# Kernel tuning notes

Measured on AMD Instinct MI355X. Metric: run time of the kernel, lower is better.

Reference implementation:

```python
import jax, jax.numpy as jnp
import numpy as np

B, L, D, O = 4, 256, 512, 128

def setup_inputs() -> dict:
    key = jax.random.key(0)
    k1, k2, k3, k4, k5, k6 = jax.random.split(key, 6)
    return {
        "x1": jax.random.normal(k1, (B, L, D), jnp.float32),
        "x2": jax.random.normal(k2, (B, L, D), jnp.float32),
        "bw": jax.random.uniform(k3, (2,), jnp.float32),
        "W_bil": jax.random.normal(k4, (O, D + 1, D + 1), jnp.float32) * 0.02,
        "W_lin": jax.random.normal(k5, (2 * D, O), jnp.float32) * 0.02,
        "b_lin": jax.random.normal(k6, (O,), jnp.float32) * 0.02,
    }

def reference(x1, x2, bw, W_bil, W_lin, b_lin):
    bwn = jax.nn.softmax(bw)
    d1 = x1.shape[-1]
    # Bilinear with bias_x/bias_y: append ones column to x1 and x2.
    ones1 = jnp.ones((*x1.shape[:2], 1), x1.dtype)
    ones2 = jnp.ones((*x2.shape[:2], 1), x2.dtype)
    x1b = jnp.concatenate([x1, ones1], axis=-1)  # [B, L1, D+1]
    x2b = jnp.concatenate([x2, ones2], axis=-1)  # [B, L2, D+1]
    # einsum 'bxi,oij,byj->boxy' then permute(0,2,3,1) -> bxyo
    bilinear_logits = jnp.einsum('bxi,oij,byj->bxyo', x1b, W_bil, x2b)
    # linear over concat([x1 expanded, x2 expanded]) == split-weight broadcast sum
    lin1 = x1 @ W_lin[:d1]   # [B, L1, O]
    lin2 = x2 @ W_lin[d1:]   # [B, L2, O]
    linear_logits = lin1[:, :, None, :] + lin2[:, None, :, :] + b_lin  # [B, L1, L2, O]
    return bwn[0] * bilinear_logits + bwn[1] * linear_logits
```

## Files before the change

### kernel.cpp

```cpp
#include <hip/hip_runtime.h>


#define LL 256
#define DD 512
#define OO 128
#define BB 4
#define WB_OI 263169
#define WB_R512 262656

typedef __attribute__((ext_vector_type(8))) short  short8;
typedef __attribute__((ext_vector_type(8))) unsigned short us8;
typedef __attribute__((ext_vector_type(4))) unsigned short us4;
typedef __attribute__((ext_vector_type(4))) float  f32x4;

__device__ __forceinline__ unsigned short f2bf(float f) {
    unsigned int u = __builtin_bit_cast(unsigned int, f);
    u = (u + 0x7FFFu + ((u >> 16) & 1u)) >> 16;
    return (unsigned short)u;
}
__device__ __forceinline__ float bf2f(unsigned short s) {
    return __builtin_bit_cast(float, (unsigned int)s << 16);
}
__device__ __forceinline__ void load_lds16(const void* g, void* l) {
    __builtin_amdgcn_global_load_lds(
        (const __attribute__((address_space(1))) unsigned int*)g,
        (__attribute__((address_space(3))) unsigned int*)l, 16, 0, 0);
}

__global__ __launch_bounds__(256) void cast_kernel(
    const float* __restrict__ src, unsigned short* __restrict__ dst, int n4)
{
    int i = blockIdx.x * 256 + threadIdx.x;
    if (i < n4) {
        float4 v = ((const float4*)src)[i];
        us4 u; u.x = f2bf(v.x); u.y = f2bf(v.y); u.z = f2bf(v.z); u.w = f2bf(v.w);
        *(us4*)(dst + (size_t)i * 4) = u;
    }
}

__global__ __launch_bounds__(256) void prepw_kernel(
    const float* __restrict__ Wb, const float* __restrict__ bw,
    unsigned short* __restrict__ Wb16)
{
    const int t = threadIdx.x;
    const int row = blockIdx.x * 4 + (t >> 6);
    const int o = row >> 9, i = row & 511;
    const int l = t & 63;
    const float e0 = __expf(bw[0]), e1 = __expf(bw[1]);
    const float bwn0 = e0 / (e0 + e1);
    const float* src = Wb + (size_t)o * WB_OI + (size_t)i * 513 + l * 8;
    float4 v0 = *(const float4*)src;
    float4 v1 = *(const float4*)(src + 4);
    us8 u;
    u[0] = f2bf(bwn0 * v0.x); u[1] = f2bf(bwn0 * v0.y);
    u[2] = f2bf(bwn0 * v0.z); u[3] = f2bf(bwn0 * v0.w);
    u[4] = f2bf(bwn0 * v1.x); u[5] = f2bf(bwn0 * v1.y);
    u[6] = f2bf(bwn0 * v1.z); u[7] = f2bf(bwn0 * v1.w);
    *(us8*)(Wb16 + (size_t)row * 512 + l * 8) = u;
}

__global__ __launch_bounds__(128) void u512_kernel(
    const float* __restrict__ x2, const float* __restrict__ Wb,
    const float* __restrict__ W_lin, const float* __restrict__ b_lin,
    const float* __restrict__ bw, float* __restrict__ u512buf)
{
    __shared__ float xs[DD];
    const int by = blockIdx.x;
    const int o  = threadIdx.x;
    const float* xr = x2 + (size_t)by * DD;
    for (int j = o; j < DD; j += 128) xs[j] = xr[j];
    __syncthreads();
    const float* W2 = Wb + (size_t)o * WB_OI + WB_R512;
    float s1 = W2[512];
    float s2 = b_lin[o];
    for (int j = 0; j < DD; ++j) {
        s1 += xs[j] * W2[j];
        s2 += xs[j] * W_lin[(size_t)(DD + j) * OO + o];
    }
    const float e0 = __expf(bw[0]), e1 = __expf(bw[1]);
    const float bwn0 = e0 / (e0 + e1), bwn1 = e1 / (e0 + e1);
    u512buf[(size_t)by * OO + o] = bwn0 * s1 + bwn1 * s2;
}

__global__ __launch_bounds__(256) void passA_kernel(
    const unsigned short* __restrict__ x2b, const unsigned short* __restrict__ Wb16,
    const float* __restrict__ W_bil, const float* __restrict__ W_lin,
    const float* __restrict__ bw, unsigned short* __restrict__ Up, int b)
{
    __shared__ __align__(16) char smem[18432];
    unsigned short* As = (unsigned short*)smem;
    unsigned short* Bs = (unsigned short*)(smem + 8192);
    unsigned short* Cs = (unsigned short*)smem;
    float* corr = (float*)(smem + 17408);

    const int t = threadIdx.x, w = t >> 6, l = t & 63;
    const int ib = blockIdx.x * 128;
    const int yb = blockIdx.y * 128;
    const int o  = blockIdx.z;
    const int wy = w & 1, wx = w >> 1;

    f32x4 acc[4][4] = {};
    const unsigned short* Wo16 = Wb16 + (size_t)o * DD * DD;

    for (int kt = 0; kt < 16; ++kt) {
        const int k0 = kt * 32;
        #pragma unroll
        for (int q = 0; q < 2; ++q) {
            const int rb = w * 32 + q * 16;
            const int rr = rb + (l >> 2);
            const int ko = k0 + (l & 3) * 8;
            load_lds16(x2b + (size_t)(b * LL + yb + rr) * DD + ko, As + rb * 32);
            load_lds16(Wo16 + (size_t)(ib + rr) * DD + ko, Bs + rb * 32);
        }
        __syncthreads();
        short8 af[4], bf[4];
        const int mrow = wy * 64 + (l & 15);
        const int ncol = wx * 64 + (l & 15);
        const int kg = (l >> 4) * 8;
        #pragma unroll
        for (int mt = 0; mt < 4; ++mt) af[mt] = *(const short8*)(As + (mrow + mt * 16) * 32 + kg);
        #pragma unroll
        for (int nt = 0; nt < 4; ++nt) bf[nt] = *(const short8*)(Bs + (ncol + nt * 16) * 32 + kg);
        #pragma unroll
        for (int mt = 0; mt < 4; ++mt)
            #pragma unroll
            for (int nt = 0; nt < 4; ++nt)
                acc[mt][nt] = __builtin_amdgcn_mfma_f32_16x16x32_bf16(af[mt], bf[nt], acc[mt][nt], 0, 0, 0);
        __syncthreads();
    }

    const float e0 = __expf(bw[0]), e1 = __expf(bw[1]);
    const float bwn0 = e0 / (e0 + e1), bwn1 = e1 / (e0 + e1);
    if (t < 128) {
        const int ig = ib + t;
        corr[t] = bwn1 * W_lin[(size_t)ig * OO + o]
                + bwn0 * W_bil[(size_t)o * WB_OI + (size_t)ig * 513 + 512];
    }
    #pragma unroll
    for (int half = 0; half < 2; ++half) {
        if (wy == half) {
            #pragma unroll
            for (int mt = 0; mt < 4; ++mt) {
                const int yl = mt * 16 + ((l >> 4) << 2);
                #pragma unroll
                for (int nt = 0; nt < 4; ++nt) {
                    const int ic = wx * 64 + nt * 16 + (l & 15);
                    #pragma unroll
                    for (int r = 0; r < 4; ++r)
                        Cs[(yl + r) * 136 + ic] = f2bf(acc[mt][nt][r]);
                }
            }
        }
        __syncthreads();
        #pragma unroll
        for (int p = 0; p < 4; ++p) {
            const int yl = p * 16 + (t >> 4);
            const int i0 = (t & 15) * 8;
            short8 v = *(const short8*)(Cs + yl * 136 + i0);
            us8 uo;
            #pragma unroll
            for (int e = 0; e < 8; ++e)
                uo[e] = f2bf(bf2f((unsigned short)v[e]) + corr[i0 + e]);
            *(us8*)(Up + ((size_t)(yb + half * 64 + yl) * OO + o) * DD + ib + i0) = uo;
        }
        __syncthreads();
    }
}

__global__ __launch_bounds__(256) void passB_kernel(
    const unsigned short* __restrict__ x1b, const unsigned short* __restrict__ Up,
    const float* __restrict__ u512buf, float* __restrict__ out, int b)
{
    __shared__ unsigned short As[128 * 32];
    __shared__ unsigned short Bs[128 * 32];
    __shared__ float u5[128];
    const int t = threadIdx.x, w = t >> 6, l = t & 63;
    const int xb = blockIdx.x * 128;
    const int y  = blockIdx.y;
    const int wy = w & 1, wx = w >> 1;
    if (t < 128) u5[t] = u512buf[(size_t)(b * LL + y) * OO + t];

    f32x4 acc[4][4] = {};

    for (int kt = 0; kt < 16; ++kt) {
        const int k0 = kt * 32;
        #pragma unroll
        for (int q = 0; q < 2; ++q) {
            const int rb = w * 32 + q * 16;
            const int rr = rb + (l >> 2);
            const int ko = k0 + (l & 3) * 8;
            load_lds16(x1b + (size_t)(b * LL + xb + rr) * DD + ko, As + rb * 32);
            load_lds16(Up + (size_t)(y * OO + rr) * DD + ko, Bs + rb * 32);
        }
        __syncthreads();
        short8 af[4], bf[4];
        const int mrow = wy * 64 + (l & 15);
        const int ncol = wx * 64 + (l & 15);
        const int kg = (l >> 4) * 8;
        #pragma unroll
        for (int mt = 0; mt < 4; ++mt) af[mt] = *(const short8*)(As + (mrow + mt * 16) * 32 + kg);
        #pragma unroll
        for (int nt = 0; nt < 4; ++nt) bf[nt] = *(const short8*)(Bs + (ncol + nt * 16) * 32 + kg);
        #pragma unroll
        for (int mt = 0; mt < 4; ++mt)
            #pragma unroll
            for (int nt = 0; nt < 4; ++nt)
                acc[mt][nt] = __builtin_amdgcn_mfma_f32_16x16x32_bf16(af[mt], bf[nt], acc[mt][nt], 0, 0, 0);
        __syncthreads();
    }

    #pragma unroll
    for (int mt = 0; mt < 4; ++mt) {
        const int xr = wy * 64 + mt * 16 + ((l >> 4) << 2);
        #pragma unroll
        for (int nt = 0; nt < 4; ++nt) {
            const int oc = wx * 64 + nt * 16 + (l & 15);
            const float c = u5[oc];
            #pragma unroll
            for (int r = 0; r < 4; ++r)
                out[((size_t)(b * LL + xb + xr + r) * LL + y) * OO + oc] = acc[mt][nt][r] + c;
        }
    }
}

extern "C" void kernel_launch(void* const* d_in, const int* in_sizes, int n_in,
                              void* d_out, int out_size, void* d_ws, size_t ws_size,
                              hipStream_t stream)
{
    const float* x1    = (const float*)d_in[0];
    const float* x2    = (const float*)d_in[1];
    const float* bw    = (const float*)d_in[2];
    const float* W_bil = (const float*)d_in[3];
    const float* W_lin = (const float*)d_in[4];
    const float* b_lin = (const float*)d_in[5];
    float* out = (float*)d_out;

    char* ws = (char*)d_ws;
    unsigned short* x1b16 = (unsigned short*)ws;
    unsigned short* x2b16 = (unsigned short*)(ws + (1u << 20));
    float*          u512b = (float*)(ws + (2u << 20));
    unsigned short* Wb16  = (unsigned short*)(ws + (3u << 20));
    unsigned short* Up    = (unsigned short*)(ws + (3u << 20) + ((size_t)128 * 512 * 512 * 2));

    cast_kernel<<<512, 256, 0, stream>>>(x1, x1b16, 131072);
    cast_kernel<<<512, 256, 0, stream>>>(x2, x2b16, 131072);
    prepw_kernel<<<16384, 256, 0, stream>>>(W_bil, bw, Wb16);
    u512_kernel<<<BB * LL, 128, 0, stream>>>(x2, W_bil, W_lin, b_lin, bw, u512b);

    for (int b = 0; b < BB; ++b) {
        passA_kernel<<<dim3(4, 2, OO), 256, 0, stream>>>(x2b16, Wb16, W_bil, W_lin, bw, Up, b);
        passB_kernel<<<dim3(2, LL), 256, 0, stream>>>(x1b16, Up, u512b, out, b);
    }
}
```

Baseline: 504.4 us.

## Batch passA/passB over all batches, double-buffer LDS, coalesce weight prep

Launches passA and passB once over all batches instead of looping per batch, which gives larger grids and removes per-batch launch serialization. Both GEMM kernels now double-buffer their LDS tiles so the next K-slice loads while the current one is multiplied. prepw uses coalesced scalar loads and stores instead of misaligned float4 loads, and the last-row bilinear weights are transposed once so u512 reads them coalesced. The two cast kernels are merged into one launch. In exchange the Up workspace grows to cover all batches, which adds memory footprint and traffic, and the larger LDS footprint may reduce occupancy.

New measurement: 479.8 us. -4.9%, faster.

```diff
diff --git a/kernel.cpp b/kernel.cpp
--- a/kernel.cpp
+++ b/kernel.cpp
@@ -27,15 +27,17 @@
         (__attribute__((address_space(3))) unsigned int*)l, 16, 0, 0);
 }
 
-__global__ __launch_bounds__(256) void cast_kernel(
-    const float* __restrict__ src, unsigned short* __restrict__ dst, int n4)
+__global__ __launch_bounds__(256) void cast2_kernel(
+    const float* __restrict__ x1, const float* __restrict__ x2,
+    unsigned short* __restrict__ x1b, unsigned short* __restrict__ x2b)
 {
     int i = blockIdx.x * 256 + threadIdx.x;
-    if (i < n4) {
-        float4 v = ((const float4*)src)[i];
-        us4 u; u.x = f2bf(v.x); u.y = f2bf(v.y); u.z = f2bf(v.z); u.w = f2bf(v.w);
-        *(us4*)(dst + (size_t)i * 4) = u;
-    }
+    const float* s; unsigned short* d; int j;
+    if (i < 131072) { s = x1; d = x1b; j = i; }
+    else            { s = x2; d = x2b; j = i - 131072; }
+    float4 v = ((const float4*)s)[j];
+    us4 u; u.x = f2bf(v.x); u.y = f2bf(v.y); u.z = f2bf(v.z); u.w = f2bf(v.w);
+    *(us4*)(d + (size_t)j * 4) = u;
 }
 
 __global__ __launch_bounds__(256) void prepw_kernel(
@@ -48,19 +50,27 @@
     const int l = t & 63;
     const float e0 = __expf(bw[0]), e1 = __expf(bw[1]);
     const float bwn0 = e0 / (e0 + e1);
-    const float* src = Wb + (size_t)o * WB_OI + (size_t)i * 513 + l * 8;
-    float4 v0 = *(const float4*)src;
-    float4 v1 = *(const float4*)(src + 4);
-    us8 u;
-    u[0] = f2bf(bwn0 * v0.x); u[1] = f2bf(bwn0 * v0.y);
-    u[2] = f2bf(bwn0 * v0.z); u[3] = f2bf(bwn0 * v0.w);
-    u[4] = f2bf(bwn0 * v1.x); u[5] = f2bf(bwn0 * v1.y);
-    u[6] = f2bf(bwn0 * v1.z); u[7] = f2bf(bwn0 * v1.w);
-    *(us8*)(Wb16 + (size_t)row * 512 + l * 8) = u;
+    const float* src = Wb + (size_t)o * WB_OI + (size_t)i * 513;
+    unsigned short* dst = Wb16 + (size_t)row * 512;
+    float v[8];
+    #pragma unroll
+    for (int e = 0; e < 8; ++e) v[e] = src[e * 64 + l];
+    #pragma unroll
+    for (int e = 0; e < 8; ++e) dst[e * 64 + l] = f2bf(bwn0 * v[e]);
+}
+
+__global__ __launch_bounds__(256) void prep512_kernel(
+    const float* __restrict__ Wb, float* __restrict__ W512T)
+{
+    int idx = blockIdx.x * 256 + threadIdx.x;
+    if (idx < 513 * 128) {
+        const int o = idx & 127, j = idx >> 7;
+        W512T[idx] = Wb[(size_t)o * WB_OI + WB_R512 + j];
+    }
 }
 
 __global__ __launch_bounds__(128) void u512_kernel(
-    const float* __restrict__ x2, const float* __restrict__ Wb,
+    const float* __restrict__ x2, const float* __restrict__ W512T,
     const float* __restrict__ W_lin, const float* __restrict__ b_lin,
     const float* __restrict__ bw, float* __restrict__ u512buf)
 {
@@ -70,11 +80,11 @@
     const float* xr = x2 + (size_t)by * DD;
     for (int j = o; j < DD; j += 128) xs[j] = xr[j];
     __syncthreads();
-    const float* W2 = Wb + (size_t)o * WB_OI + WB_R512;
-    float s1 = W2[512];
+    float s1 = W512T[512 * 128 + o];
     float s2 = b_lin[o];
+    #pragma unroll 4
     for (int j = 0; j < DD; ++j) {
-        s1 += xs[j] * W2[j];
+        s1 += xs[j] * W512T[j * 128 + o];
         s2 += xs[j] * W_lin[(size_t)(DD + j) * OO + o];
     }
     const float e0 = __expf(bw[0]), e1 = __expf(bw[1]);
@@ -85,49 +95,65 @@
 __global__ __launch_bounds__(256) void passA_kernel(
     const unsigned short* __restrict__ x2b, const unsigned short* __restrict__ Wb16,
     const float* __restrict__ W_bil, const float* __restrict__ W_lin,
-    const float* __restrict__ bw, unsigned short* __restrict__ Up, int b)
-{
-    __shared__ __align__(16) char smem[18432];
-    unsigned short* As = (unsigned short*)smem;
-    unsigned short* Bs = (unsigned short*)(smem + 8192);
-    unsigned short* Cs = (unsigned short*)smem;
-    float* corr = (float*)(smem + 17408);
+    const float* __restrict__ bw, unsigned short* __restrict__ Up)
+{
+    __shared__ __align__(16) char smem[33280];
+    unsigned short* As0 = (unsigned short*)smem;
+    unsigned short* Bs0 = (unsigned short*)(smem + 8192);
+    unsigned short* As1 = (unsigned short*)(smem + 16384);
+    unsigned short* Bs1 = (unsigned short*)(smem + 24576);
+    unsigned short* Cs  = (unsigned short*)smem;
+    float* corr = (float*)(smem + 32768);
 
     const int t = threadIdx.x, w = t >> 6, l = t & 63;
     const int ib = blockIdx.x * 128;
-    const int yb = blockIdx.y * 128;
+    const int yg = blockIdx.y * 128;
     const int o  = blockIdx.z;
     const int wy = w & 1, wx = w >> 1;
 
     f32x4 acc[4][4] = {};
     const unsigned short* Wo16 = Wb16 + (size_t)o * DD * DD;
 
+    const int rb0 = w * 32;
+    const int rr  = l >> 2;
+    const int kof = (l & 3) * 8;
+
+#define STAGE_A(ASP, BSP, K0) do {                                              \
+    _Pragma("unroll")                                                           \
+    for (int q = 0; q < 2; ++q) {                                               \
+        const int rb = rb0 + q * 16, rrow = rb + rr, ko = (K0) + kof;           \
+        load_lds16(x2b  + (size_t)(yg + rrow) * DD + ko, (ASP) + rb * 32);      \
+        load_lds16(Wo16 + (size_t)(ib + rrow) * DD + ko, (BSP) + rb * 32);      \
+    } } while (0)
+
+    STAGE_A(As0, Bs0, 0);
+    __syncthreads();
+
+    const int mrow = wy * 64 + (l & 15);
+    const int ncol = wx * 64 + (l & 15);
+    const int kg = (l >> 4) * 8;
+
+    #pragma unroll 2
     for (int kt = 0; kt < 16; ++kt) {
-        const int k0 = kt * 32;
-        #pragma unroll
-        for (int q = 0; q < 2; ++q) {
-            const int rb = w * 32 + q * 16;
-            const int rr = rb + (l >> 2);
-            const int ko = k0 + (l & 3) * 8;
-            load_lds16(x2b + (size_t)(b * LL + yb + rr) * DD + ko, As + rb * 32);
-            load_lds16(Wo16 + (size_t)(ib + rr) * DD + ko, Bs + rb * 32);
-        }
-        __syncthreads();
-        short8 af[4], bf[4];
-        const int mrow = wy * 64 + (l & 15);
-        const int ncol = wx * 64 + (l & 15);
-        const int kg = (l >> 4) * 8;
-        #pragma unroll
-        for (int mt = 0; mt < 4; ++mt) af[mt] = *(const short8*)(As + (mrow + mt * 16) * 32 + kg);
-        #pragma unroll
-        for (int nt = 0; nt < 4; ++nt) bf[nt] = *(const short8*)(Bs + (ncol + nt * 16) * 32 + kg);
+        const int cur = kt & 1;
+        unsigned short* Asr = cur ? As1 : As0;
+        unsigned short* Bsr = cur ? Bs1 : Bs0;
+        unsigned short* Asn = cur ? As0 : As1;
+        unsigned short* Bsn = cur ? Bs0 : Bs1;
+        if (kt < 15) STAGE_A(Asn, Bsn, (kt + 1) * 32);
+        short8 af[4], bfr[4];
+        #pragma unroll
+        for (int mt = 0; mt < 4; ++mt) af[mt]  = *(const short8*)(Asr + (mrow + mt * 16) * 32 + kg);
+        #pragma unroll
+        for (int nt = 0; nt < 4; ++nt) bfr[nt] = *(const short8*)(Bsr + (ncol + nt * 16) * 32 + kg);
         #pragma unroll
         for (int mt = 0; mt < 4; ++mt)
             #pragma unroll
             for (int nt = 0; nt < 4; ++nt)
-                acc[mt][nt] = __builtin_amdgcn_mfma_f32_16x16x32_bf16(af[mt], bf[nt], acc[mt][nt], 0, 0, 0);
-        __syncthreads();
-    }
+                acc[mt][nt] = __builtin_amdgcn_mfma_f32_16x16x32_bf16(af[mt], bfr[nt], acc[mt][nt], 0, 0, 0);
+        __syncthreads();
+    }
+#undef STAGE_A
 
     const float e0 = __expf(bw[0]), e1 = __expf(bw[1]);
     const float bwn0 = e0 / (e0 + e1), bwn1 = e1 / (e0 + e1);
@@ -161,7 +187,7 @@
             #pragma unroll
             for (int e = 0; e < 8; ++e)
                 uo[e] = f2bf(bf2f((unsigned short)v[e]) + corr[i0 + e]);
-            *(us8*)(Up + ((size_t)(yb + half * 64 + yl) * OO + o) * DD + ib + i0) = uo;
+            *(us8*)(Up + ((size_t)(yg + half * 64 + yl) * OO + o) * DD + ib + i0) = uo;
         }
         __syncthreads();
     }
@@ -169,45 +195,64 @@
 
 __global__ __launch_bounds__(256) void passB_kernel(
     const unsigned short* __restrict__ x1b, const unsigned short* __restrict__ Up,
-    const float* __restrict__ u512buf, float* __restrict__ out, int b)
-{
-    __shared__ unsigned short As[128 * 32];
-    __shared__ unsigned short Bs[128 * 32];
-    __shared__ float u5[128];
+    const float* __restrict__ u512buf, float* __restrict__ out)
+{
+    __shared__ __align__(16) char smem[33280];
+    unsigned short* As0 = (unsigned short*)smem;
+    unsigned short* Bs0 = (unsigned short*)(smem + 8192);
+    unsigned short* As1 = (unsigned short*)(smem + 16384);
+    unsigned short* Bs1 = (unsigned short*)(smem + 24576);
+    float* u5 = (float*)(smem + 32768);
+
     const int t = threadIdx.x, w = t >> 6, l = t & 63;
     const int xb = blockIdx.x * 128;
-    const int y  = blockIdx.y;
+    const int yg = blockIdx.y;
+    const int bb = yg >> 8, y = yg & 255;
     const int wy = w & 1, wx = w >> 1;
-    if (t < 128) u5[t] = u512buf[(size_t)(b * LL + y) * OO + t];
+    if (t < 128) u5[t] = u512buf[(size_t)yg * OO + t];
 
     f32x4 acc[4][4] = {};
 
+    const int rb0 = w * 32;
+    const int rr  = l >> 2;
+    const int kof = (l & 3) * 8;
+
+#define STAGE_B(ASP, BSP, K0) do {                                                   \
+    _Pragma("unroll")                                                                \
+    for (int q = 0; q < 2; ++q) {                                                    \
+        const int rb = rb0 + q * 16, rrow = rb + rr, ko = (K0) + kof;                \
+        load_lds16(x1b + (size_t)(bb * LL + xb + rrow) * DD + ko, (ASP) + rb * 32);  \
+        load_lds16(Up  + (size_t)(yg * OO + rrow) * DD + ko,      (BSP) + rb * 32);  \
+    } } while (0)
+
+    STAGE_B(As0, Bs0, 0);
+    __syncthreads();
+
+    const int mrow = wy * 64 + (l & 15);
+    const int ncol = wx * 64 + (l & 15);
+    const int kg = (l >> 4) * 8;
+
+    #pragma unroll 2
     for (int kt = 0; kt < 16; ++kt) {
-        const int k0 = kt * 32;
-        #pragma unroll
-        for (int q = 0; q < 2; ++q) {
-            const int rb = w * 32 + q * 16;
-            const int rr = rb + (l >> 2);
-            const int ko = k0 + (l & 3) * 8;
-            load_lds16(x1b + (size_t)(b * LL + xb + rr) * DD + ko, As + rb * 32);
-            load_lds16(Up + (size_t)(y * OO + rr) * DD + ko, Bs + rb * 32);
-        }
-        __syncthreads();
-        short8 af[4], bf[4];
-        const int mrow = wy * 64 + (l & 15);
-        const int ncol = wx * 64 + (l & 15);
-        const int kg = (l >> 4) * 8;
-        #pragma unroll
-        for (int mt = 0; mt < 4; ++mt) af[mt] = *(const short8*)(As + (mrow + mt * 16) * 32 + kg);
-        #pragma unroll
-        for (int nt = 0; nt < 4; ++nt) bf[nt] = *(const short8*)(Bs + (ncol + nt * 16) * 32 + kg);
+        const int cur = kt & 1;
+        unsigned short* Asr = cur ? As1 : As0;
+        unsigned short* Bsr = cur ? Bs1 : Bs0;
+        unsigned short* Asn = cur ? As0 : As1;
+        unsigned short* Bsn = cur ? Bs0 : Bs1;
+        if (kt < 15) STAGE_B(Asn, Bsn, (kt + 1) * 32);
+        short8 af[4], bfr[4];
+        #pragma unroll
+        for (int mt = 0; mt < 4; ++mt) af[mt]  = *(const short8*)(Asr + (mrow + mt * 16) * 32 + kg);
+        #pragma unroll
+        for (int nt = 0; nt < 4; ++nt) bfr[nt] = *(const short8*)(Bsr + (ncol + nt * 16) * 32 + kg);
         #pragma unroll
         for (int mt = 0; mt < 4; ++mt)
             #pragma unroll
             for (int nt = 0; nt < 4; ++nt)
-                acc[mt][nt] = __builtin_amdgcn_mfma_f32_16x16x32_bf16(af[mt], bf[nt], acc[mt][nt], 0, 0, 0);
-        __syncthreads();
-    }
+                acc[mt][nt] = __builtin_amdgcn_mfma_f32_16x16x32_bf16(af[mt], bfr[nt], acc[mt][nt], 0, 0, 0);
+        __syncthreads();
+    }
+#undef STAGE_B
 
     #pragma unroll
     for (int mt = 0; mt < 4; ++mt) {
@@ -218,7 +263,7 @@
             const float c = u5[oc];
             #pragma unroll
             for (int r = 0; r < 4; ++r)
-                out[((size_t)(b * LL + xb + xr + r) * LL + y) * OO + oc] = acc[mt][nt][r] + c;
+                out[((size_t)(bb * LL + xb + xr + r) * LL + y) * OO + oc] = acc[mt][nt][r] + c;
         }
     }
 }
@@ -239,16 +284,15 @@
     unsigned short* x1b16 = (unsigned short*)ws;
     unsigned short* x2b16 = (unsigned short*)(ws + (1u << 20));
     float*          u512b = (float*)(ws + (2u << 20));
+    float*          W512T = (float*)(ws + (2u << 20) + (512u << 10));
     unsigned short* Wb16  = (unsigned short*)(ws + (3u << 20));
     unsigned short* Up    = (unsigned short*)(ws + (3u << 20) + ((size_t)128 * 512 * 512 * 2));
 
-    cast_kernel<<<512, 256, 0, stream>>>(x1, x1b16, 131072);
-    cast_kernel<<<512, 256, 0, stream>>>(x2, x2b16, 131072);
+    cast2_kernel<<<1024, 256, 0, stream>>>(x1, x2, x1b16, x2b16);
     prepw_kernel<<<16384, 256, 0, stream>>>(W_bil, bw, Wb16);
-    u512_kernel<<<BB * LL, 128, 0, stream>>>(x2, W_bil, W_lin, b_lin, bw, u512b);
-
-    for (int b = 0; b < BB; ++b) {
-        passA_kernel<<<dim3(4, 2, OO), 256, 0, stream>>>(x2b16, Wb16, W_bil, W_lin, bw, Up, b);
-        passB_kernel<<<dim3(2, LL), 256, 0, stream>>>(x1b16, Up, u512b, out, b);
-    }
-}
+    prep512_kernel<<<257, 256, 0, stream>>>(W_bil, W512T);
+    u512_kernel<<<BB * LL, 128, 0, stream>>>(x2, W512T, W_lin, b_lin, bw, u512b);
+
+    passA_kernel<<<dim3(4, 8, OO), 256, 0, stream>>>(x2b16, Wb16, W_bil, W_lin, bw, Up);
+    passB_kernel<<<dim3(2, BB * LL), 256, 0, stream>>>(x1b16, Up, u512b, out);
+}
```
